# Kernel optimization log

Measured on AMD Instinct MI355X. Metric: run time of the kernel, lower is better.

Reference implementation:

```python
import jax, jax.numpy as jnp
import numpy as np

N_NODES = 20000
N_EDGES = 640000
IN_CH = 64
EDGE_DIM = 16
HID = 128
N_LAYERS = 3
OUT_DIM = 1
N_GRAPHS = 128


def setup_inputs() -> dict:
    key = jax.random.key(0)
    ks = jax.random.split(key, 20)

    def w(k, shape, fan_in):
        return jax.random.normal(k, shape, dtype=jnp.float32) / np.sqrt(fan_in)

    inp = {
        'x': jax.random.normal(ks[0], (N_NODES, IN_CH), dtype=jnp.float32),
        'edge_index': jax.random.randint(ks[1], (2, N_EDGES), 0, N_NODES),
        'edge_attr': jax.random.normal(ks[2], (N_EDGES, EDGE_DIM), dtype=jnp.float32),
        'batch': jnp.sort(jax.random.randint(ks[3], (N_NODES,), 0, N_GRAPHS)),
        # node projection
        'node_proj_w': w(ks[4], (IN_CH, HID), IN_CH),
        'node_proj_b': jnp.zeros((HID,), jnp.float32),
        # stacked per-layer params [L, ...]
        'msg_w1': w(ks[5], (N_LAYERS, HID + EDGE_DIM, HID), HID + EDGE_DIM),
        'msg_b1': jnp.zeros((N_LAYERS, HID), jnp.float32),
        'msg_w2': w(ks[6], (N_LAYERS, HID, HID), HID),
        'msg_b2': jnp.zeros((N_LAYERS, HID), jnp.float32),
        'upd_w': w(ks[7], (N_LAYERS, HID + HID, HID), HID + HID),
        'upd_b': jnp.zeros((N_LAYERS, HID), jnp.float32),
        'ln_g': jnp.ones((N_LAYERS, HID), jnp.float32),
        'ln_b': jnp.zeros((N_LAYERS, HID), jnp.float32),
        # readout FFNN
        'ffn_w1': w(ks[8], (2 * HID, HID), 2 * HID),
        'ffn_b1': jnp.zeros((HID,), jnp.float32),
        'ffn_w2': w(ks[9], (HID, OUT_DIM), HID),
        'ffn_b2': jnp.zeros((OUT_DIM,), jnp.float32),
    }
    return inp


def _layernorm(h, g, b, eps=1e-5):
    mu = jnp.mean(h, axis=-1, keepdims=True)
    var = jnp.var(h, axis=-1, keepdims=True)
    return (h - mu) * jax.lax.rsqrt(var + eps) * g + b


def reference(x, edge_index, edge_attr, batch,
              node_proj_w, node_proj_b,
              msg_w1, msg_b1, msg_w2, msg_b2,
              upd_w, upd_b, ln_g, ln_b,
              ffn_w1, ffn_b1, ffn_w2, ffn_b2):
    src = edge_index[0]  # x_j (source nodes, default PyG flow)
    dst = edge_index[1]  # aggregation target

    h = x @ node_proj_w + node_proj_b  # [N, HID]

    for l in range(N_LAYERS):
        h_res = h
        # message MLP per edge: cat([x_j, edge_attr]) -> Linear,ReLU,Linear
        ej = jnp.concatenate([h[src], edge_attr], axis=-1)  # [E, HID+EDGE_DIM]
        m = jax.nn.relu(ej @ msg_w1[l] + msg_b1[l]) @ msg_w2[l] + msg_b2[l]
        # scatter-add aggregate
        aggr = jax.ops.segment_sum(m, dst, num_segments=N_NODES)  # [N, HID]
        # update MLP: cat([x, aggr]) -> Linear,ReLU; then LayerNorm
        u = jax.nn.relu(jnp.concatenate([h, aggr], axis=-1) @ upd_w[l] + upd_b[l])
        u = _layernorm(u, ln_g[l], ln_b[l])
        # relu, (dropout = identity in eval), residual
        h = jax.nn.relu(u) + h_res

    # global mean / max pooling per graph
    counts = jax.ops.segment_sum(jnp.ones((h.shape[0], 1), h.dtype), batch,
                                 num_segments=N_GRAPHS)
    x_mean = jax.ops.segment_sum(h, batch, num_segments=N_GRAPHS) / jnp.maximum(counts, 1.0)
    x_max = jax.ops.segment_max(h, batch, num_segments=N_GRAPHS)
    g = jnp.concatenate([x_mean, x_max], axis=1)  # [G, 2*HID]

    out = jax.nn.relu(g @ ffn_w1 + ffn_b1) @ ffn_w2 + ffn_b2  # [G, OUT_DIM]
    return out
```

## Files before the change

kernel.cpp:

```cpp
#include <hip/hip_runtime.h>
#include <hip/hip_fp16.h>
#include <math.h>

#define N_NODES 20000
#define N_EDGES 640000
#define IN_CH 64
#define EDGE_DIM 16
#define HID 128
#define N_LAYERS 3
#define N_GRAPHS 128

typedef _Float16 h2 __attribute__((ext_vector_type(2)));

__device__ inline float fdot2f(h2 a, h2 b, float c) {
#if __has_builtin(__builtin_amdgcn_fdot2)
    return __builtin_amdgcn_fdot2(a, b, c, false);
#else
    float d;
    asm("v_dot2_f32_f16 %0, %1, %2, %3" : "=v"(d) : "v"(a), "v"(b), "v"(c));
    return d;
#endif
}


__global__ void hist_kernel(const int* __restrict__ dst, int* __restrict__ deg, int n) {
    int i = blockIdx.x * blockDim.x + threadIdx.x;
    if (i < n) atomicAdd(&deg[dst[i]], 1);
}

__global__ __launch_bounds__(1024) void scan_kernel(const int* __restrict__ deg,
                                                    int* __restrict__ rowptr) {
    __shared__ int buf[1024];
    const int t = threadIdx.x;
    constexpr int PER = 20;
    const int base = t * PER;
    int loc[PER];
    int s = 0;
    #pragma unroll
    for (int i = 0; i < PER; i++) {
        int v = (base + i < N_NODES) ? deg[base + i] : 0;
        loc[i] = s; s += v;
    }
    buf[t] = s;
    __syncthreads();
    for (int off = 1; off < 1024; off <<= 1) {
        int x = (t >= off) ? buf[t - off] : 0;
        __syncthreads();
        buf[t] += x;
        __syncthreads();
    }
    const int excl = (t == 0) ? 0 : buf[t - 1];
    #pragma unroll
    for (int i = 0; i < PER; i++)
        if (base + i < N_NODES) rowptr[base + i] = excl + loc[i];
    if (t == 1023) rowptr[N_NODES] = buf[1023];
}

__global__ __launch_bounds__(256) void scatter_kernel(const int* __restrict__ ei,
                                                      const float* __restrict__ ea,
                                                      const int* __restrict__ rowptr,
                                                      int* __restrict__ cursor,
                                                      int* __restrict__ csr_src,
                                                      __half* __restrict__ eattr, int n) {
    int e = blockIdx.x * blockDim.x + threadIdx.x;
    if (e < n) {
        int d = ei[N_EDGES + e];
        int pos = atomicAdd(&cursor[d], 1);
        int slot = rowptr[d] + pos;
        csr_src[slot] = ei[e];
        const float4* s4 = (const float4*)(ea + (size_t)e * EDGE_DIM);
        const float4 a = s4[0], b = s4[1], c = s4[2], dd = s4[3];
        union { uint4 u; __half2 h[4]; } p0, p1;
        p0.h[0] = __floats2half2_rn(a.x, a.y);  p0.h[1] = __floats2half2_rn(a.z, a.w);
        p0.h[2] = __floats2half2_rn(b.x, b.y);  p0.h[3] = __floats2half2_rn(b.z, b.w);
        p1.h[0] = __floats2half2_rn(c.x, c.y);  p1.h[1] = __floats2half2_rn(c.z, c.w);
        p1.h[2] = __floats2half2_rn(dd.x, dd.y); p1.h[3] = __floats2half2_rn(dd.z, dd.w);
        uint4* o = (uint4*)(eattr + (size_t)slot * EDGE_DIM);
        o[0] = p0.u; o[1] = p1.u;
    }
}

__global__ __launch_bounds__(128) void prep_w1e(const float* __restrict__ msg_w1,
                                                __half2* __restrict__ pk) {
    const int l = blockIdx.x, c = threadIdx.x;
    const float* W1e = msg_w1 + (size_t)l * (HID + EDGE_DIM) * HID + HID * HID;
    #pragma unroll
    for (int j = 0; j < 8; j++) {
        __half2 v = __floats2half2_rn(W1e[(2 * j) * HID + c], W1e[(2 * j + 1) * HID + c]);
        pk[((l * 8 + j) * 64 + (c >> 1)) * 2 + (c & 1)] = v;
    }
}


template<int KIN, bool HALF_OUT>
__global__ __launch_bounds__(128) void gemm_nodes(const float* __restrict__ in,
                                                  const float* __restrict__ W,
                                                  const float* __restrict__ bias,
                                                  void* __restrict__ outp) {
    constexpr int NPB = 16;
    __shared__ __align__(16) float a[NPB * KIN];
    const int t = threadIdx.x;
    const int node0 = blockIdx.x * NPB;
    const float* src = in + (size_t)node0 * KIN;
    #pragma unroll
    for (int i = t * 4; i < NPB * KIN; i += 512)
        *(float4*)(a + i) = *(const float4*)(src + i);
    __syncthreads();
    float acc[NPB];
    const float bv = bias[t];
    #pragma unroll
    for (int n = 0; n < NPB; n++) acc[n] = bv;
    for (int k = 0; k < KIN; k += 4) {
        const float w0 = W[(k + 0) * HID + t];
        const float w1 = W[(k + 1) * HID + t];
        const float w2 = W[(k + 2) * HID + t];
        const float w3 = W[(k + 3) * HID + t];
        #pragma unroll
        for (int n = 0; n < NPB; n++) {
            const float4 av = *(const float4*)(a + n * KIN + k);
            acc[n] += av.x * w0 + av.y * w1 + av.z * w2 + av.w * w3;
        }
    }
    if (HALF_OUT) {
        __half* o = (__half*)outp + (size_t)node0 * HID + t;
        #pragma unroll
        for (int n = 0; n < NPB; n++) o[n * HID] = __float2half(acc[n]);
    } else {
        float* o = (float*)outp + (size_t)node0 * HID + t;
        #pragma unroll
        for (int n = 0; n < NPB; n++) o[n * HID] = acc[n];
    }
}


__global__ __launch_bounds__(128) void w2u_all(const float* __restrict__ msg_w2,
                                               const float* __restrict__ msg_b2,
                                               const float* __restrict__ upd_w,
                                               float* __restrict__ W2u,
                                               float* __restrict__ b2u) {
    __shared__ float row[HID];
    const int t = threadIdx.x;
    const int l = blockIdx.x / 129, d = blockIdx.x % 129;
    const float* w2 = msg_w2 + (size_t)l * HID * HID;
    const float* wu_bot = upd_w + (size_t)l * 2 * HID * HID + HID * HID;
    const float* src = (d < HID) ? (w2 + d * HID) : (msg_b2 + l * HID);
    row[t] = src[t];
    __syncthreads();
    float acc = 0.f;
    for (int k = 0; k < HID; k++) acc += row[k] * wu_bot[k * HID + t];
    if (d < HID) W2u[(size_t)l * HID * HID + d * HID + t] = acc;
    else b2u[l * HID + t] = acc;
}


__global__ __launch_bounds__(256) void edge_aggr4(const __half* __restrict__ npart,
                                                  const __half2* __restrict__ w1epk,
                                                  const __half* __restrict__ eattr,
                                                  const int* __restrict__ rowptr,
                                                  const int* __restrict__ csr_src,
                                                  float* __restrict__ r) {
    const int t = threadIdx.x;
    const int w = t >> 6, l = t & 63;
    const int node = blockIdx.x * 4 + w;
    h2 wk0[8], wk1[8];
    const uint2* wp = (const uint2*)w1epk;
    #pragma unroll
    for (int j = 0; j < 8; j++) {
        union { uint u; h2 h; } q0, q1;
        const uint2 q = wp[j * 64 + l];
        q0.u = q.x; q1.u = q.y;
        wk0[j] = q0.h; wk1[j] = q1.h;
    }
    const int beg = rowptr[node], end = rowptr[node + 1];
    float acc0 = 0.f, acc1 = 0.f;
    int i = beg;
    for (; i + 4 <= end; i += 4) {
        int s[4];
        #pragma unroll
        for (int j = 0; j < 4; j++) s[j] = csr_src[i + j];
        h2 hv[4];
        #pragma unroll
        for (int j = 0; j < 4; j++)
            hv[j] = *(const h2*)(npart + (size_t)s[j] * HID + 2 * l);
        #pragma unroll
        for (int j = 0; j < 4; j++) {
            union { uint4 u; h2 h[4]; } ea, eb;
            const uint4* ep = (const uint4*)(eattr + (size_t)(i + j) * EDGE_DIM);
            ea.u = ep[0]; eb.u = ep[1];
            float z0 = (float)hv[j].x, z1 = (float)hv[j].y;
            #pragma unroll
            for (int k = 0; k < 4; k++) {
                z0 = fdot2f(ea.h[k], wk0[k], z0);
                z1 = fdot2f(ea.h[k], wk1[k], z1);
            }
            #pragma unroll
            for (int k = 0; k < 4; k++) {
                z0 = fdot2f(eb.h[k], wk0[4 + k], z0);
                z1 = fdot2f(eb.h[k], wk1[4 + k], z1);
            }
            acc0 += fmaxf(z0, 0.f);
            acc1 += fmaxf(z1, 0.f);
        }
    }
    for (; i < end; i++) {
        const int s0 = csr_src[i];
        const h2 hv0 = *(const h2*)(npart + (size_t)s0 * HID + 2 * l);
        union { uint4 u; h2 h[4]; } ea, eb;
        const uint4* ep = (const uint4*)(eattr + (size_t)i * EDGE_DIM);
        ea.u = ep[0]; eb.u = ep[1];
        float z0 = (float)hv0.x, z1 = (float)hv0.y;
        #pragma unroll
        for (int k = 0; k < 4; k++) {
            z0 = fdot2f(ea.h[k], wk0[k], z0);
            z1 = fdot2f(ea.h[k], wk1[k], z1);
        }
        #pragma unroll
        for (int k = 0; k < 4; k++) {
            z0 = fdot2f(eb.h[k], wk0[4 + k], z0);
            z1 = fdot2f(eb.h[k], wk1[4 + k], z1);
        }
        acc0 += fmaxf(z0, 0.f);
        acc1 += fmaxf(z1, 0.f);
    }
    *(float2*)(r + (size_t)node * HID + 2 * l) = make_float2(acc0, acc1);
}


template<bool EMIT>
__global__ __launch_bounds__(128) void update_nodes(float* __restrict__ h,
                                                    const float* __restrict__ r,
                                                    const int* __restrict__ deg,
                                                    const float* __restrict__ Wt,
                                                    const float* __restrict__ W2u,
                                                    const float* __restrict__ ub,
                                                    const float* __restrict__ b2u,
                                                    const float* __restrict__ lng,
                                                    const float* __restrict__ lnb,
                                                    const float* __restrict__ nw1,
                                                    const float* __restrict__ nb1,
                                                    __half* __restrict__ npart) {
    constexpr int NPB = 16;
    __shared__ __align__(16) float sh[NPB * HID];
    __shared__ __align__(16) float sr[NPB * HID];
    __shared__ float smu[NPB], srs[NPB];
    const int t = threadIdx.x;
    const int node0 = blockIdx.x * NPB;
    #pragma unroll
    for (int i = t * 4; i < NPB * HID; i += 512) {
        *(float4*)(sh + i) = *(const float4*)(h + (size_t)node0 * HID + i);
        *(float4*)(sr + i) = *(const float4*)(r + (size_t)node0 * HID + i);
    }
    __syncthreads();
    float acc[NPB];
    const float ubv = ub[t], b2uv = b2u[t];
    #pragma unroll
    for (int n = 0; n < NPB; n++) acc[n] = ubv + (float)deg[node0 + n] * b2uv;
    for (int k = 0; k < HID; k += 4) {
        const float wt0 = Wt[(k + 0) * HID + t], w20 = W2u[(k + 0) * HID + t];
        const float wt1 = Wt[(k + 1) * HID + t], w21 = W2u[(k + 1) * HID + t];
        const float wt2 = Wt[(k + 2) * HID + t], w22 = W2u[(k + 2) * HID + t];
        const float wt3 = Wt[(k + 3) * HID + t], w23 = W2u[(k + 3) * HID + t];
        #pragma unroll
        for (int n = 0; n < NPB; n++) {
            const float4 hv = *(const float4*)(sh + n * HID + k);
            const float4 rv = *(const float4*)(sr + n * HID + k);
            acc[n] += hv.x * wt0 + hv.y * wt1 + hv.z * wt2 + hv.w * wt3;
            acc[n] += rv.x * w20 + rv.y * w21 + rv.z * w22 + rv.w * w23;
        }
    }
    #pragma unroll
    for (int n = 0; n < NPB; n++) acc[n] = fmaxf(acc[n], 0.f);
    __syncthreads();
    #pragma unroll
    for (int n = 0; n < NPB; n++) sr[n * HID + t] = acc[n];
    __syncthreads();
    {
        const int n = t >> 3, lane = t & 7;
        float s = 0.f, ss = 0.f;
        #pragma unroll
        for (int i = 0; i < 16; i++) {
            float v = sr[n * HID + lane + i * 8];
            s += v; ss += v * v;
        }
        s += __shfl_xor(s, 1); ss += __shfl_xor(ss, 1);
        s += __shfl_xor(s, 2); ss += __shfl_xor(ss, 2);
        s += __shfl_xor(s, 4); ss += __shfl_xor(ss, 4);
        if (lane == 0) {
            float mu = s * (1.f / HID);
            float var = ss * (1.f / HID) - mu * mu;
            smu[n] = mu;
            srs[n] = rsqrtf(var + 1e-5f);
        }
    }
    __syncthreads();
    const float g = lng[t], b = lnb[t];
    #pragma unroll
    for (int n = 0; n < NPB; n++) {
        float v = (acc[n] - smu[n]) * srs[n] * g + b;
        v = fmaxf(v, 0.f) + sh[n * HID + t];
        acc[n] = v;
        h[(size_t)(node0 + n) * HID + t] = v;
    }
    if (EMIT) {
        __syncthreads();
        #pragma unroll
        for (int n = 0; n < NPB; n++) sh[n * HID + t] = acc[n];
        __syncthreads();
        float acc2[NPB];
        const float nbv = nb1[t];
        #pragma unroll
        for (int n = 0; n < NPB; n++) acc2[n] = nbv;
        for (int k = 0; k < HID; k += 4) {
            const float w0 = nw1[(k + 0) * HID + t];
            const float w1 = nw1[(k + 1) * HID + t];
            const float w2 = nw1[(k + 2) * HID + t];
            const float w3 = nw1[(k + 3) * HID + t];
            #pragma unroll
            for (int n = 0; n < NPB; n++) {
                const float4 hv = *(const float4*)(sh + n * HID + k);
                acc2[n] += hv.x * w0 + hv.y * w1 + hv.z * w2 + hv.w * w3;
            }
        }
        __half* o = npart + (size_t)node0 * HID + t;
        #pragma unroll
        for (int n = 0; n < NPB; n++) o[n * HID] = __float2half(acc2[n]);
    }
}


__global__ __launch_bounds__(128) void pool_readout(const float* __restrict__ h,
                                                    const int* __restrict__ batch,
                                                    const float* __restrict__ w1,
                                                    const float* __restrict__ b1,
                                                    const float* __restrict__ w2,
                                                    const float* __restrict__ b2,
                                                    float* __restrict__ out) {
    __shared__ int sbe[2];
    __shared__ float g[2 * HID];
    __shared__ float red[2];
    const int t = threadIdx.x, gi = blockIdx.x;
    if (t < 2) {
        const int target = gi + t;
        int lo = 0, hi = N_NODES;
        while (lo < hi) { int m = (lo + hi) >> 1; if (batch[m] < target) lo = m + 1; else hi = m; }
        sbe[t] = lo;
    }
    __syncthreads();
    const int beg = sbe[0], end = sbe[1];
    float sum = 0.f, mx = -INFINITY;
    int n = beg;
    for (; n + 4 <= end; n += 4) {
        const float v0 = h[(size_t)(n + 0) * HID + t];
        const float v1 = h[(size_t)(n + 1) * HID + t];
        const float v2 = h[(size_t)(n + 2) * HID + t];
        const float v3 = h[(size_t)(n + 3) * HID + t];
        sum += v0 + v1 + v2 + v3;
        mx = fmaxf(mx, fmaxf(fmaxf(v0, v1), fmaxf(v2, v3)));
    }
    for (; n < end; n++) { const float v = h[(size_t)n * HID + t]; sum += v; mx = fmaxf(mx, v); }
    const float c = fmaxf((float)(end - beg), 1.f);
    g[t] = sum / c;
    g[HID + t] = mx;
    __syncthreads();
    float acc = b1[t];
    for (int k = 0; k < 2 * HID; k++) acc += g[k] * w1[k * HID + t];
    float s = fmaxf(acc, 0.f) * w2[t];
    s += __shfl_down(s, 32); s += __shfl_down(s, 16); s += __shfl_down(s, 8);
    s += __shfl_down(s, 4);  s += __shfl_down(s, 2);  s += __shfl_down(s, 1);
    if ((t & 63) == 0) red[t >> 6] = s;
    __syncthreads();
    if (t == 0) out[gi] = red[0] + red[1] + b2[0];
}


extern "C" void kernel_launch(void* const* d_in, const int* in_sizes, int n_in,
                              void* d_out, int out_size, void* d_ws, size_t ws_size,
                              hipStream_t stream) {
    const float* x           = (const float*)d_in[0];
    const int*   edge_index  = (const int*)  d_in[1];
    const float* edge_attr   = (const float*)d_in[2];
    const int*   batch       = (const int*)  d_in[3];
    const float* node_proj_w = (const float*)d_in[4];
    const float* node_proj_b = (const float*)d_in[5];
    const float* msg_w1      = (const float*)d_in[6];
    const float* msg_b1      = (const float*)d_in[7];
    const float* msg_w2      = (const float*)d_in[8];
    const float* msg_b2      = (const float*)d_in[9];
    const float* upd_w       = (const float*)d_in[10];
    const float* upd_b       = (const float*)d_in[11];
    const float* ln_g        = (const float*)d_in[12];
    const float* ln_b        = (const float*)d_in[13];
    const float* ffn_w1      = (const float*)d_in[14];
    const float* ffn_b1      = (const float*)d_in[15];
    const float* ffn_w2      = (const float*)d_in[16];
    const float* ffn_b2      = (const float*)d_in[17];
    float* out = (float*)d_out;

    char* ws = (char*)d_ws;
    size_t off = 0;
    auto alloc = [&](size_t b) -> char* {
        char* p = ws + off;
        off = (off + b + 255) & ~(size_t)255;
        return p;
    };
    float*    h        = (float*)alloc((size_t)N_NODES * HID * 4);
    __half*   npart_h  = (__half*)alloc((size_t)N_NODES * HID * 2);
    float*    r        = (float*)alloc((size_t)N_NODES * HID * 4);
    float*    W2u_all  = (float*)alloc((size_t)N_LAYERS * HID * HID * 4);
    float*    b2u_all  = (float*)alloc((size_t)N_LAYERS * HID * 4);
    __half2*  w1epk    = (__half2*)alloc((size_t)N_LAYERS * 8 * 64 * 2 * 4);
    int*      rowptr   = (int*)alloc((N_NODES + 1) * 4);
    int*      deg      = (int*)alloc((size_t)N_NODES * 4 * 2);
    int*      cursor   = deg + N_NODES;
    int*      csr_src  = (int*)alloc((size_t)N_EDGES * 4);
    __half*   eattr_h  = (__half*)alloc((size_t)N_EDGES * EDGE_DIM * 2);
    (void)in_sizes; (void)n_in; (void)out_size; (void)ws_size;

    hipMemsetAsync(deg, 0, (size_t)N_NODES * 4 * 2, stream);
    hist_kernel<<<(N_EDGES + 255) / 256, 256, 0, stream>>>(edge_index + N_EDGES, deg, N_EDGES);
    scan_kernel<<<1, 1024, 0, stream>>>(deg, rowptr);
    scatter_kernel<<<(N_EDGES + 255) / 256, 256, 0, stream>>>(edge_index, edge_attr, rowptr,
                                                              cursor, csr_src, eattr_h, N_EDGES);
    prep_w1e<<<N_LAYERS, 128, 0, stream>>>(msg_w1, w1epk);
    w2u_all<<<N_LAYERS * 129, 128, 0, stream>>>(msg_w2, msg_b2, upd_w, W2u_all, b2u_all);
    gemm_nodes<IN_CH, false><<<N_NODES / 16, 128, 0, stream>>>(x, node_proj_w, node_proj_b, h);
    gemm_nodes<HID, true><<<N_NODES / 16, 128, 0, stream>>>(h, msg_w1, msg_b1, npart_h);

    for (int l = 0; l < N_LAYERS; l++) {
        edge_aggr4<<<N_NODES / 4, 256, 0, stream>>>(npart_h, w1epk + (size_t)l * 8 * 64 * 2,
                                                    eattr_h, rowptr, csr_src, r);
        const bool emit = (l + 1 < N_LAYERS);
        const float* nw1 = msg_w1 + (size_t)(l + 1) * (HID + EDGE_DIM) * HID;
        const float* nb1 = msg_b1 + (size_t)(l + 1) * HID;
        if (emit)
            update_nodes<true><<<N_NODES / 16, 128, 0, stream>>>(
                h, r, deg, upd_w + (size_t)l * 2 * HID * HID,
                W2u_all + (size_t)l * HID * HID, upd_b + l * HID, b2u_all + l * HID,
                ln_g + l * HID, ln_b + l * HID, nw1, nb1, npart_h);
        else
            update_nodes<false><<<N_NODES / 16, 128, 0, stream>>>(
                h, r, deg, upd_w + (size_t)l * 2 * HID * HID,
                W2u_all + (size_t)l * HID * HID, upd_b + l * HID, b2u_all + l * HID,
                ln_g + l * HID, ln_b + l * HID, nullptr, nullptr, nullptr);
    }

    pool_readout<<<N_GRAPHS, 128, 0, stream>>>(h, batch, ffn_w1, ffn_b1, ffn_w2, ffn_b2, out);
}
```

Baseline: 615.5 us.

## Split node features into channel planes and use fp16 dot2 in node update

The fp16 node projection buffer is stored as two 64-channel planes. The edge aggregation kernel now has each block process one plane for a group of nodes, with a block-index swizzle so the two planes of the same nodes run close together, and it reads edge attributes and CSR indices with nontemporal loads. The node update GEMMs pack weights into half2 form with a new pack kernel, hold h and r as fp16 in shared memory, and accumulate with v_dot2. Layernorm now uses wave shuffles, and the update uses 8 nodes per block. This targets gather traffic and ALU cost in the update kernels, at the cost of fp16 rounding of h and r inside the update GEMM and twice as many edge-kernel blocks, each of which re-reads the CSR indices and edge attributes.

```diff
diff --git a/kernel.cpp b/kernel.cpp
--- a/kernel.cpp
+++ b/kernel.cpp
@@ -9,8 +9,10 @@
 #define HID 128
 #define N_LAYERS 3
 #define N_GRAPHS 128
+#define PLANE ((size_t)N_NODES * 64)
 
 typedef _Float16 h2 __attribute__((ext_vector_type(2)));
+typedef unsigned long long ull;
 
 __device__ inline float fdot2f(h2 a, h2 b, float c) {
 #if __has_builtin(__builtin_amdgcn_fdot2)
@@ -20,6 +22,10 @@
     asm("v_dot2_f32_f16 %0, %1, %2, %3" : "=v"(d) : "v"(a), "v"(b), "v"(c));
     return d;
 #endif
+}
+__device__ inline h2 asH2(unsigned u) { union { unsigned u; h2 h; } x; x.u = u; return x.h; }
+__device__ inline unsigned packh2(float a, float b) {
+    union { __half2 h; unsigned u; } x; x.h = __floats2half2_rn(a, b); return x.u;
 }
 
 
@@ -70,66 +76,23 @@
         csr_src[slot] = ei[e];
         const float4* s4 = (const float4*)(ea + (size_t)e * EDGE_DIM);
         const float4 a = s4[0], b = s4[1], c = s4[2], dd = s4[3];
-        union { uint4 u; __half2 h[4]; } p0, p1;
-        p0.h[0] = __floats2half2_rn(a.x, a.y);  p0.h[1] = __floats2half2_rn(a.z, a.w);
-        p0.h[2] = __floats2half2_rn(b.x, b.y);  p0.h[3] = __floats2half2_rn(b.z, b.w);
-        p1.h[0] = __floats2half2_rn(c.x, c.y);  p1.h[1] = __floats2half2_rn(c.z, c.w);
-        p1.h[2] = __floats2half2_rn(dd.x, dd.y); p1.h[3] = __floats2half2_rn(dd.z, dd.w);
+        uint4 p0, p1;
+        p0.x = packh2(a.x, a.y);  p0.y = packh2(a.z, a.w);
+        p0.z = packh2(b.x, b.y);  p0.w = packh2(b.z, b.w);
+        p1.x = packh2(c.x, c.y);  p1.y = packh2(c.z, c.w);
+        p1.z = packh2(dd.x, dd.y); p1.w = packh2(dd.z, dd.w);
         uint4* o = (uint4*)(eattr + (size_t)slot * EDGE_DIM);
-        o[0] = p0.u; o[1] = p1.u;
+        o[0] = p0; o[1] = p1;
     }
 }
 
 __global__ __launch_bounds__(128) void prep_w1e(const float* __restrict__ msg_w1,
-                                                __half2* __restrict__ pk) {
+                                                unsigned* __restrict__ pk) {
     const int l = blockIdx.x, c = threadIdx.x;
     const float* W1e = msg_w1 + (size_t)l * (HID + EDGE_DIM) * HID + HID * HID;
     #pragma unroll
-    for (int j = 0; j < 8; j++) {
-        __half2 v = __floats2half2_rn(W1e[(2 * j) * HID + c], W1e[(2 * j + 1) * HID + c]);
-        pk[((l * 8 + j) * 64 + (c >> 1)) * 2 + (c & 1)] = v;
-    }
-}
-
-
-template<int KIN, bool HALF_OUT>
-__global__ __launch_bounds__(128) void gemm_nodes(const float* __restrict__ in,
-                                                  const float* __restrict__ W,
-                                                  const float* __restrict__ bias,
-                                                  void* __restrict__ outp) {
-    constexpr int NPB = 16;
-    __shared__ __align__(16) float a[NPB * KIN];
-    const int t = threadIdx.x;
-    const int node0 = blockIdx.x * NPB;
-    const float* src = in + (size_t)node0 * KIN;
-    #pragma unroll
-    for (int i = t * 4; i < NPB * KIN; i += 512)
-        *(float4*)(a + i) = *(const float4*)(src + i);
-    __syncthreads();
-    float acc[NPB];
-    const float bv = bias[t];
-    #pragma unroll
-    for (int n = 0; n < NPB; n++) acc[n] = bv;
-    for (int k = 0; k < KIN; k += 4) {
-        const float w0 = W[(k + 0) * HID + t];
-        const float w1 = W[(k + 1) * HID + t];
-        const float w2 = W[(k + 2) * HID + t];
-        const float w3 = W[(k + 3) * HID + t];
-        #pragma unroll
-        for (int n = 0; n < NPB; n++) {
-            const float4 av = *(const float4*)(a + n * KIN + k);
-            acc[n] += av.x * w0 + av.y * w1 + av.z * w2 + av.w * w3;
-        }
-    }
-    if (HALF_OUT) {
-        __half* o = (__half*)outp + (size_t)node0 * HID + t;
-        #pragma unroll
-        for (int n = 0; n < NPB; n++) o[n * HID] = __float2half(acc[n]);
-    } else {
-        float* o = (float*)outp + (size_t)node0 * HID + t;
-        #pragma unroll
-        for (int n = 0; n < NPB; n++) o[n * HID] = acc[n];
-    }
+    for (int j = 0; j < 8; j++)
+        pk[((size_t)l * HID + c) * 8 + j] = packh2(W1e[(2 * j) * HID + c], W1e[(2 * j + 1) * HID + c]);
 }
 
 
@@ -152,178 +115,238 @@
     else b2u[l * HID + t] = acc;
 }
 
-
-__global__ __launch_bounds__(256) void edge_aggr4(const __half* __restrict__ npart,
-                                                  const __half2* __restrict__ w1epk,
+__global__ __launch_bounds__(128) void pack_upd(const float* __restrict__ upd_w,
+                                                const float* __restrict__ W2u_all,
+                                                const float* __restrict__ msg_w1,
+                                                unsigned* __restrict__ pkU) {
+    const int id = blockIdx.x;
+    const int l = id / 3, m = id % 3, c = threadIdx.x;
+    unsigned* dst = pkU + (size_t)id * 16 * 128 * 4;
+    const float* src;
+    if (m == 0) src = upd_w + (size_t)l * 2 * HID * HID;
+    else if (m == 1) src = W2u_all + (size_t)l * HID * HID;
+    else { if (l == 2) return; src = msg_w1 + (size_t)(l + 1) * (HID + EDGE_DIM) * HID; }
+    for (int k2 = 0; k2 < 64; k2++) {
+        const int kk = k2 >> 2, q = k2 & 3;
+        dst[((size_t)kk * 128 + c) * 4 + q] = packh2(src[(2 * k2) * HID + c],
+                                                     src[(2 * k2 + 1) * HID + c]);
+    }
+}
+
+
+template<int KIN, bool HALF_OUT>
+__global__ __launch_bounds__(128) void gemm_nodes(const float* __restrict__ in,
+                                                  const float* __restrict__ W,
+                                                  const float* __restrict__ bias,
+                                                  void* __restrict__ outp) {
+    constexpr int NPB = 16;
+    __shared__ __align__(16) float a[NPB * KIN];
+    const int t = threadIdx.x;
+    const int node0 = blockIdx.x * NPB;
+    const float* src = in + (size_t)node0 * KIN;
+    #pragma unroll
+    for (int i = t * 4; i < NPB * KIN; i += 512)
+        *(float4*)(a + i) = *(const float4*)(src + i);
+    __syncthreads();
+    float acc[NPB];
+    const float bv = bias[t];
+    #pragma unroll
+    for (int n = 0; n < NPB; n++) acc[n] = bv;
+    for (int k = 0; k < KIN; k += 4) {
+        const float w0 = W[(k + 0) * HID + t];
+        const float w1 = W[(k + 1) * HID + t];
+        const float w2 = W[(k + 2) * HID + t];
+        const float w3 = W[(k + 3) * HID + t];
+        #pragma unroll
+        for (int n = 0; n < NPB; n++) {
+            const float4 av = *(const float4*)(a + n * KIN + k);
+            acc[n] += av.x * w0 + av.y * w1 + av.z * w2 + av.w * w3;
+        }
+    }
+    if (HALF_OUT) {
+        __half* o = (__half*)outp + (size_t)(t >> 6) * PLANE + (size_t)node0 * 64 + (t & 63);
+        #pragma unroll
+        for (int n = 0; n < NPB; n++) o[n * 64] = __float2half(acc[n]);
+    } else {
+        float* o = (float*)outp + (size_t)node0 * HID + t;
+        #pragma unroll
+        for (int n = 0; n < NPB; n++) o[n * HID] = acc[n];
+    }
+}
+
+
+__global__ __launch_bounds__(256) void edge_aggr5(const __half* __restrict__ npart,
+                                                  const unsigned* __restrict__ w1epk,
                                                   const __half* __restrict__ eattr,
                                                   const int* __restrict__ rowptr,
                                                   const int* __restrict__ csr_src,
                                                   float* __restrict__ r) {
-    const int t = threadIdx.x;
-    const int w = t >> 6, l = t & 63;
-    const int node = blockIdx.x * 4 + w;
-    h2 wk0[8], wk1[8];
-    const uint2* wp = (const uint2*)w1epk;
-    #pragma unroll
-    for (int j = 0; j < 8; j++) {
-        union { uint u; h2 h; } q0, q1;
-        const uint2 q = wp[j * 64 + l];
-        q0.u = q.x; q1.u = q.y;
-        wk0[j] = q0.h; wk1[j] = q1.h;
-    }
+    const int bid = blockIdx.x;
+    const int t = threadIdx.x, w = t >> 6, l = t & 63;
+    const int pass = (bid >> 2) & 1;
+    const int node = (((bid >> 3) << 2) + (bid & 3)) * 4 + w;
+    const int ch = pass * 64 + l;
+    h2 wk[8];
+    {
+        const uint4* wp = (const uint4*)(w1epk + (size_t)ch * 8);
+        const uint4 w0 = wp[0], w1 = wp[1];
+        wk[0] = asH2(w0.x); wk[1] = asH2(w0.y); wk[2] = asH2(w0.z); wk[3] = asH2(w0.w);
+        wk[4] = asH2(w1.x); wk[5] = asH2(w1.y); wk[6] = asH2(w1.z); wk[7] = asH2(w1.w);
+    }
+    const __half* np = npart + (size_t)pass * PLANE;
     const int beg = rowptr[node], end = rowptr[node + 1];
-    float acc0 = 0.f, acc1 = 0.f;
+    float acc = 0.f;
     int i = beg;
     for (; i + 4 <= end; i += 4) {
         int s[4];
         #pragma unroll
-        for (int j = 0; j < 4; j++) s[j] = csr_src[i + j];
-        h2 hv[4];
-        #pragma unroll
-        for (int j = 0; j < 4; j++)
-            hv[j] = *(const h2*)(npart + (size_t)s[j] * HID + 2 * l);
+        for (int j = 0; j < 4; j++) s[j] = __builtin_nontemporal_load(csr_src + i + j);
+        float hv[4];
+        #pragma unroll
+        for (int j = 0; j < 4; j++) hv[j] = __half2float(np[(size_t)s[j] * 64 + l]);
         #pragma unroll
         for (int j = 0; j < 4; j++) {
-            union { uint4 u; h2 h[4]; } ea, eb;
-            const uint4* ep = (const uint4*)(eattr + (size_t)(i + j) * EDGE_DIM);
-            ea.u = ep[0]; eb.u = ep[1];
-            float z0 = (float)hv[j].x, z1 = (float)hv[j].y;
+            union { ull v[4]; h2 h[8]; } ea;
+            const ull* p = (const ull*)(eattr + (size_t)(i + j) * EDGE_DIM);
+            ea.v[0] = __builtin_nontemporal_load(p + 0);
+            ea.v[1] = __builtin_nontemporal_load(p + 1);
+            ea.v[2] = __builtin_nontemporal_load(p + 2);
+            ea.v[3] = __builtin_nontemporal_load(p + 3);
+            float z = hv[j];
             #pragma unroll
-            for (int k = 0; k < 4; k++) {
-                z0 = fdot2f(ea.h[k], wk0[k], z0);
-                z1 = fdot2f(ea.h[k], wk1[k], z1);
-            }
-            #pragma unroll
-            for (int k = 0; k < 4; k++) {
-                z0 = fdot2f(eb.h[k], wk0[4 + k], z0);
-                z1 = fdot2f(eb.h[k], wk1[4 + k], z1);
-            }
-            acc0 += fmaxf(z0, 0.f);
-            acc1 += fmaxf(z1, 0.f);
+            for (int k = 0; k < 8; k++) z = fdot2f(ea.h[k], wk[k], z);
+            acc += fmaxf(z, 0.f);
         }
     }
     for (; i < end; i++) {
-        const int s0 = csr_src[i];
-        const h2 hv0 = *(const h2*)(npart + (size_t)s0 * HID + 2 * l);
-        union { uint4 u; h2 h[4]; } ea, eb;
-        const uint4* ep = (const uint4*)(eattr + (size_t)i * EDGE_DIM);
-        ea.u = ep[0]; eb.u = ep[1];
-        float z0 = (float)hv0.x, z1 = (float)hv0.y;
-        #pragma unroll
-        for (int k = 0; k < 4; k++) {
-            z0 = fdot2f(ea.h[k], wk0[k], z0);
-            z1 = fdot2f(ea.h[k], wk1[k], z1);
-        }
-        #pragma unroll
-        for (int k = 0; k < 4; k++) {
-            z0 = fdot2f(eb.h[k], wk0[4 + k], z0);
-            z1 = fdot2f(eb.h[k], wk1[4 + k], z1);
-        }
-        acc0 += fmaxf(z0, 0.f);
-        acc1 += fmaxf(z1, 0.f);
-    }
-    *(float2*)(r + (size_t)node * HID + 2 * l) = make_float2(acc0, acc1);
+        const int s0 = __builtin_nontemporal_load(csr_src + i);
+        const float hv0 = __half2float(np[(size_t)s0 * 64 + l]);
+        union { ull v[4]; h2 h[8]; } ea;
+        const ull* p = (const ull*)(eattr + (size_t)i * EDGE_DIM);
+        ea.v[0] = __builtin_nontemporal_load(p + 0);
+        ea.v[1] = __builtin_nontemporal_load(p + 1);
+        ea.v[2] = __builtin_nontemporal_load(p + 2);
+        ea.v[3] = __builtin_nontemporal_load(p + 3);
+        float z = hv0;
+        #pragma unroll
+        for (int k = 0; k < 8; k++) z = fdot2f(ea.h[k], wk[k], z);
+        acc += fmaxf(z, 0.f);
+    }
+    r[(size_t)node * HID + ch] = acc;
 }
 
 
 template<bool EMIT>
-__global__ __launch_bounds__(128) void update_nodes(float* __restrict__ h,
-                                                    const float* __restrict__ r,
-                                                    const int* __restrict__ deg,
-                                                    const float* __restrict__ Wt,
-                                                    const float* __restrict__ W2u,
-                                                    const float* __restrict__ ub,
-                                                    const float* __restrict__ b2u,
-                                                    const float* __restrict__ lng,
-                                                    const float* __restrict__ lnb,
-                                                    const float* __restrict__ nw1,
-                                                    const float* __restrict__ nb1,
-                                                    __half* __restrict__ npart) {
-    constexpr int NPB = 16;
-    __shared__ __align__(16) float sh[NPB * HID];
-    __shared__ __align__(16) float sr[NPB * HID];
-    __shared__ float smu[NPB], srs[NPB];
+__global__ __launch_bounds__(128) void update_nodes2(float* __restrict__ h,
+                                                     const float* __restrict__ r,
+                                                     const int* __restrict__ deg,
+                                                     const unsigned* __restrict__ pkL,
+                                                     const float* __restrict__ ub,
+                                                     const float* __restrict__ b2u,
+                                                     const float* __restrict__ lng,
+                                                     const float* __restrict__ lnb,
+                                                     const float* __restrict__ nb1,
+                                                     __half* __restrict__ npart) {
+    constexpr int NPB = 8;
+    __shared__ unsigned sh2[NPB * 64];
+    __shared__ unsigned sr2[NPB * 64];
+    __shared__ float2 psum[2][NPB];
     const int t = threadIdx.x;
     const int node0 = blockIdx.x * NPB;
-    #pragma unroll
-    for (int i = t * 4; i < NPB * HID; i += 512) {
-        *(float4*)(sh + i) = *(const float4*)(h + (size_t)node0 * HID + i);
-        *(float4*)(sr + i) = *(const float4*)(r + (size_t)node0 * HID + i);
-    }
-    __syncthreads();
+    const float4* h4 = (const float4*)(h + (size_t)node0 * HID);
+    const float4* r4 = (const float4*)(r + (size_t)node0 * HID);
+    #pragma unroll
+    for (int i = t; i < NPB * HID / 4; i += 128) {
+        const float4 v = h4[i];
+        sh2[2 * i] = packh2(v.x, v.y); sh2[2 * i + 1] = packh2(v.z, v.w);
+        const float4 u = r4[i];
+        sr2[2 * i] = packh2(u.x, u.y); sr2[2 * i + 1] = packh2(u.z, u.w);
+    }
+    __syncthreads();
+    const unsigned* pkWt = pkL;
+    const unsigned* pkW2 = pkL + 16 * 128 * 4;
     float acc[NPB];
     const float ubv = ub[t], b2uv = b2u[t];
     #pragma unroll
     for (int n = 0; n < NPB; n++) acc[n] = ubv + (float)deg[node0 + n] * b2uv;
-    for (int k = 0; k < HID; k += 4) {
-        const float wt0 = Wt[(k + 0) * HID + t], w20 = W2u[(k + 0) * HID + t];
-        const float wt1 = Wt[(k + 1) * HID + t], w21 = W2u[(k + 1) * HID + t];
-        const float wt2 = Wt[(k + 2) * HID + t], w22 = W2u[(k + 2) * HID + t];
-        const float wt3 = Wt[(k + 3) * HID + t], w23 = W2u[(k + 3) * HID + t];
+    for (int kk = 0; kk < 16; kk++) {
+        const uint4 wt = *(const uint4*)(pkWt + ((size_t)kk * 128 + t) * 4);
+        const uint4 w2 = *(const uint4*)(pkW2 + ((size_t)kk * 128 + t) * 4);
         #pragma unroll
         for (int n = 0; n < NPB; n++) {
-            const float4 hv = *(const float4*)(sh + n * HID + k);
-            const float4 rv = *(const float4*)(sr + n * HID + k);
-            acc[n] += hv.x * wt0 + hv.y * wt1 + hv.z * wt2 + hv.w * wt3;
-            acc[n] += rv.x * w20 + rv.y * w21 + rv.z * w22 + rv.w * w23;
+            const uint4 ha = *(const uint4*)&sh2[n * 64 + kk * 4];
+            const uint4 ra = *(const uint4*)&sr2[n * 64 + kk * 4];
+            acc[n] = fdot2f(asH2(ha.x), asH2(wt.x), acc[n]);
+            acc[n] = fdot2f(asH2(ha.y), asH2(wt.y), acc[n]);
+            acc[n] = fdot2f(asH2(ha.z), asH2(wt.z), acc[n]);
+            acc[n] = fdot2f(asH2(ha.w), asH2(wt.w), acc[n]);
+            acc[n] = fdot2f(asH2(ra.x), asH2(w2.x), acc[n]);
+            acc[n] = fdot2f(asH2(ra.y), asH2(w2.y), acc[n]);
+            acc[n] = fdot2f(asH2(ra.z), asH2(w2.z), acc[n]);
+            acc[n] = fdot2f(asH2(ra.w), asH2(w2.w), acc[n]);
         }
     }
     #pragma unroll
     for (int n = 0; n < NPB; n++) acc[n] = fmaxf(acc[n], 0.f);
-    __syncthreads();
-    #pragma unroll
-    for (int n = 0; n < NPB; n++) sr[n * HID + t] = acc[n];
-    __syncthreads();
     {
-        const int n = t >> 3, lane = t & 7;
-        float s = 0.f, ss = 0.f;
-        #pragma unroll
-        for (int i = 0; i < 16; i++) {
-            float v = sr[n * HID + lane + i * 8];
-            s += v; ss += v * v;
-        }
-        s += __shfl_xor(s, 1); ss += __shfl_xor(ss, 1);
-        s += __shfl_xor(s, 2); ss += __shfl_xor(ss, 2);
-        s += __shfl_xor(s, 4); ss += __shfl_xor(ss, 4);
-        if (lane == 0) {
-            float mu = s * (1.f / HID);
-            float var = ss * (1.f / HID) - mu * mu;
-            smu[n] = mu;
-            srs[n] = rsqrtf(var + 1e-5f);
+        float s[NPB], ss[NPB];
+        #pragma unroll
+        for (int n = 0; n < NPB; n++) { s[n] = acc[n]; ss[n] = acc[n] * acc[n]; }
+        for (int off = 1; off < 64; off <<= 1) {
+            #pragma unroll
+            for (int n = 0; n < NPB; n++) {
+                s[n] += __shfl_xor(s[n], off);
+                ss[n] += __shfl_xor(ss[n], off);
+            }
+        }
+        if ((t & 63) == 0) {
+            const int wv = t >> 6;
+            #pragma unroll
+            for (int n = 0; n < NPB; n++) psum[wv][n] = make_float2(s[n], ss[n]);
         }
     }
     __syncthreads();
     const float g = lng[t], b = lnb[t];
+    float vnew[NPB];
     #pragma unroll
     for (int n = 0; n < NPB; n++) {
-        float v = (acc[n] - smu[n]) * srs[n] * g + b;
-        v = fmaxf(v, 0.f) + sh[n * HID + t];
-        acc[n] = v;
+        const float s = psum[0][n].x + psum[1][n].x;
+        const float ss = psum[0][n].y + psum[1][n].y;
+        const float mu = s * (1.f / HID);
+        const float var = ss * (1.f / HID) - mu * mu;
+        const float rs = rsqrtf(var + 1e-5f);
+        const float hold = __half2float(((const __half*)&sh2[n * 64 + (t >> 1)])[t & 1]);
+        const float v = fmaxf((acc[n] - mu) * rs * g + b, 0.f) + hold;
+        vnew[n] = v;
         h[(size_t)(node0 + n) * HID + t] = v;
     }
     if (EMIT) {
         __syncthreads();
         #pragma unroll
-        for (int n = 0; n < NPB; n++) sh[n * HID + t] = acc[n];
+        for (int n = 0; n < NPB; n++) {
+            const float vx = __shfl_xor(vnew[n], 1);
+            if (!(t & 1)) sh2[n * 64 + (t >> 1)] = packh2(vnew[n], vx);
+        }
         __syncthreads();
+        const unsigned* pkN = pkL + 2 * 16 * 128 * 4;
         float acc2[NPB];
         const float nbv = nb1[t];
         #pragma unroll
         for (int n = 0; n < NPB; n++) acc2[n] = nbv;
-        for (int k = 0; k < HID; k += 4) {
-            const float w0 = nw1[(k + 0) * HID + t];
-            const float w1 = nw1[(k + 1) * HID + t];
-            const float w2 = nw1[(k + 2) * HID + t];
-            const float w3 = nw1[(k + 3) * HID + t];
+        for (int kk = 0; kk < 16; kk++) {
+            const uint4 wn = *(const uint4*)(pkN + ((size_t)kk * 128 + t) * 4);
             #pragma unroll
             for (int n = 0; n < NPB; n++) {
-                const float4 hv = *(const float4*)(sh + n * HID + k);
-                acc2[n] += hv.x * w0 + hv.y * w1 + hv.z * w2 + hv.w * w3;
+                const uint4 ha = *(const uint4*)&sh2[n * 64 + kk * 4];
+                acc2[n] = fdot2f(asH2(ha.x), asH2(wn.x), acc2[n]);
+                acc2[n] = fdot2f(asH2(ha.y), asH2(wn.y), acc2[n]);
+                acc2[n] = fdot2f(asH2(ha.z), asH2(wn.z), acc2[n]);
+                acc2[n] = fdot2f(asH2(ha.w), asH2(wn.w), acc2[n]);
             }
         }
-        __half* o = npart + (size_t)node0 * HID + t;
-        #pragma unroll
-        for (int n = 0; n < NPB; n++) o[n * HID] = __float2half(acc2[n]);
+        __half* o = npart + (size_t)(t >> 6) * PLANE + (size_t)node0 * 64 + (t & 63);
+        #pragma unroll
+        for (int n = 0; n < NPB; n++) o[n * 64] = __float2half(acc2[n]);
     }
 }
 
@@ -404,11 +427,12 @@
         return p;
     };
     float*    h        = (float*)alloc((size_t)N_NODES * HID * 4);
-    __half*   npart_h  = (__half*)alloc((size_t)N_NODES * HID * 2);
+    __half*   npart_h  = (__half*)alloc(2 * PLANE * 2);
     float*    r        = (float*)alloc((size_t)N_NODES * HID * 4);
     float*    W2u_all  = (float*)alloc((size_t)N_LAYERS * HID * HID * 4);
     float*    b2u_all  = (float*)alloc((size_t)N_LAYERS * HID * 4);
-    __half2*  w1epk    = (__half2*)alloc((size_t)N_LAYERS * 8 * 64 * 2 * 4);
+    unsigned* w1epk    = (unsigned*)alloc((size_t)N_LAYERS * HID * 8 * 4);
+    unsigned* pkU      = (unsigned*)alloc((size_t)9 * 16 * 128 * 4 * 4);
     int*      rowptr   = (int*)alloc((N_NODES + 1) * 4);
     int*      deg      = (int*)alloc((size_t)N_NODES * 4 * 2);
     int*      cursor   = deg + N_NODES;
@@ -423,25 +447,22 @@
                                                               cursor, csr_src, eattr_h, N_EDGES);
     prep_w1e<<<N_LAYERS, 128, 0, stream>>>(msg_w1, w1epk);
     w2u_all<<<N_LAYERS * 129, 128, 0, stream>>>(msg_w2, msg_b2, upd_w, W2u_all, b2u_all);
+    pack_upd<<<9, 128, 0, stream>>>(upd_w, W2u_all, msg_w1, pkU);
     gemm_nodes<IN_CH, false><<<N_NODES / 16, 128, 0, stream>>>(x, node_proj_w, node_proj_b, h);
     gemm_nodes<HID, true><<<N_NODES / 16, 128, 0, stream>>>(h, msg_w1, msg_b1, npart_h);
 
     for (int l = 0; l < N_LAYERS; l++) {
-        edge_aggr4<<<N_NODES / 4, 256, 0, stream>>>(npart_h, w1epk + (size_t)l * 8 * 64 * 2,
+        edge_aggr5<<<N_NODES / 2, 256, 0, stream>>>(npart_h, w1epk + (size_t)l * HID * 8,
                                                     eattr_h, rowptr, csr_src, r);
-        const bool emit = (l + 1 < N_LAYERS);
-        const float* nw1 = msg_w1 + (size_t)(l + 1) * (HID + EDGE_DIM) * HID;
-        const float* nb1 = msg_b1 + (size_t)(l + 1) * HID;
-        if (emit)
-            update_nodes<true><<<N_NODES / 16, 128, 0, stream>>>(
-                h, r, deg, upd_w + (size_t)l * 2 * HID * HID,
-                W2u_all + (size_t)l * HID * HID, upd_b + l * HID, b2u_all + l * HID,
-                ln_g + l * HID, ln_b + l * HID, nw1, nb1, npart_h);
+        const unsigned* pkL = pkU + (size_t)(l * 3) * 16 * 128 * 4;
+        if (l + 1 < N_LAYERS)
+            update_nodes2<true><<<N_NODES / 8, 128, 0, stream>>>(
+                h, r, deg, pkL, upd_b + l * HID, b2u_all + l * HID,
+                ln_g + l * HID, ln_b + l * HID, msg_b1 + (size_t)(l + 1) * HID, npart_h);
         else
-            update_nodes<false><<<N_NODES / 16, 128, 0, stream>>>(
-                h, r, deg, upd_w + (size_t)l * 2 * HID * HID,
-                W2u_all + (size_t)l * HID * HID, upd_b + l * HID, b2u_all + l * HID,
-                ln_g + l * HID, ln_b + l * HID, nullptr, nullptr, nullptr);
+            update_nodes2<false><<<N_NODES / 8, 128, 0, stream>>>(
+                h, r, deg, pkL, upd_b + l * HID, b2u_all + l * HID,
+                ln_g + l * HID, ln_b + l * HID, msg_b1, npart_h);
     }
 
     pool_readout<<<N_GRAPHS, 128, 0, stream>>>(h, batch, ffn_w1, ffn_b1, ffn_w2, ffn_b2, out);
```

Result: slower. 684.6 us (+11.2%).
